# Kernel optimization log

Hardware: AMD Instinct MI355X
Metric: run time of the kernel (lower is better)

Reference implementation:

```python
import jax, jax.numpy as jnp
import numpy as np

INDEX_SHIFT = jnp.array([[0, 0], [-1, 0], [1, 0], [0, 1], [-1, 1], [1, 1], [0, -1], [-1, -1], [1, -1]], dtype=jnp.int32)
H, W = 320, 320
C = 32          # embed_dim / feat_channels (hard-coded 32 in module)
NH = 2          # head_num
HD = C // NH    # per-head dim
B, N = 4, 20000


def setup_inputs() -> dict:
    key = jax.random.key(0)
    ks = jax.random.split(key, 8)

    def coords(k):
        # unique (y, x) coords per sample so the coord->index lookup is well defined
        perm = jax.random.permutation(k, H * W)[:N]
        return jnp.stack([perm // W, perm % W], axis=-1).astype(jnp.int32)

    li_coors = jax.vmap(coords)(jax.random.split(ks[0], B))
    ra_coors = jax.vmap(coords)(jax.random.split(ks[1], B))
    li_feats = jax.random.normal(ks[2], (B, N, C), jnp.float32)
    ra_feats = jax.random.normal(ks[3], (B, N, C), jnp.float32)
    pos = jax.random.normal(ks[4], (9, C), jnp.float32) * 0.02

    s = 1.0 / np.sqrt(C)
    out = {"li_bev_feats": li_feats, "li_bev_coors": li_coors,
           "ra_bev_feats": ra_feats, "ra_bev_coors": ra_coors,
           "pos_embedding": pos}
    for i, kk in [(1, ks[5]), (2, ks[6])]:
        k0, k1 = jax.random.split(kk)
        out[f"in_w{i}"] = jax.random.uniform(k0, (3 * C, C), jnp.float32, -s, s)
        out[f"in_b{i}"] = jnp.zeros((3 * C,), jnp.float32)
        out[f"out_w{i}"] = jax.random.uniform(k1, (C, C), jnp.float32, -s, s)
        out[f"out_b{i}"] = jnp.zeros((C,), jnp.float32)
    return out


def _build_kv(q_coors, kv_coors, kv_feats, pos):
    # q_coors, kv_coors: (N,2) int; kv_feats: (N,C)
    n = q_coors.shape[0]
    grid = jnp.full((H * W,), -1, jnp.int32)
    grid = grid.at[kv_coors[:, 0] * W + kv_coors[:, 1]].set(jnp.arange(n, dtype=jnp.int32))
    sc = q_coors[None, :, :] + INDEX_SHIFT[:, None, :]            # (9,N,2)
    valid = (sc[..., 0] >= 0) & (sc[..., 0] < H) & (sc[..., 1] >= 0) & (sc[..., 1] < W)
    flat = jnp.clip(sc[..., 0], 0, H - 1) * W + jnp.clip(sc[..., 1], 0, W - 1)
    sel = jnp.where(valid, grid[flat], -1)                        # (9,N)
    mask = (sel >= 0)[..., None]                                  # (9,N,1)
    g = kv_feats[jnp.maximum(sel, 0)]                             # (9,N,C)
    k = jnp.where(mask, g, 0.0)
    v = jnp.where(mask, g + pos[:, None, :], 0.0)
    return k.transpose(1, 0, 2), v.transpose(1, 0, 2)             # (N,9,C)


def _mha(q, k, v, in_w, in_b, out_w, out_b):
    # q: (N,C); k,v: (N,L,C). torch MultiheadAttention (eval mode, dropout off).
    n, L = k.shape[0], k.shape[1]
    wq, wk, wv = in_w[:C], in_w[C:2 * C], in_w[2 * C:]
    bq, bk, bv = in_b[:C], in_b[C:2 * C], in_b[2 * C:]
    qh = (q @ wq.T + bq).reshape(n, NH, HD)
    kh = (k @ wk.T + bk).reshape(n, L, NH, HD)
    vh = (v @ wv.T + bv).reshape(n, L, NH, HD)
    scores = jnp.einsum('nhd,nlhd->nhl', qh, kh) / np.sqrt(HD)
    attn = jax.nn.softmax(scores, axis=-1)
    o = jnp.einsum('nhl,nlhd->nhd', attn, vh).reshape(n, C)
    return o @ out_w.T + out_b


def _scatter(feats, coors):
    # PointPillarsScatter: place (N,C) feats at (y,x) into a (C,H,W) canvas
    idx = coors[:, 0] * W + coors[:, 1]
    canvas = jnp.zeros((C, H * W), feats.dtype)
    return canvas.at[:, idx].set(feats.T).reshape(C, H, W)


def reference(li_bev_feats, li_bev_coors, ra_bev_feats, ra_bev_coors, pos_embedding,
              in_w1, in_b1, out_w1, out_b1, in_w2, in_b2, out_w2, out_b2):
    def one(li_f, li_c, ra_f, ra_c):
        k, v = _build_kv(li_c, ra_c, ra_f, pos_embedding)
        li_img = _scatter(_mha(li_f, k, v, in_w1, in_b1, out_w1, out_b1), li_c)
        k, v = _build_kv(ra_c, li_c, li_f, pos_embedding)
        ra_img = _scatter(_mha(ra_f, k, v, in_w2, in_b2, out_w2, out_b2), ra_c)
        return li_img, ra_img
    li_imgs, ra_imgs = jax.vmap(one)(li_bev_feats, li_bev_coors, ra_bev_feats, ra_bev_coors)
    return li_imgs, ra_imgs  # each (B, C, H, W)
```

## Files before the change

kernel.cpp:

```cpp
#include <hip/hip_runtime.h>

constexpr int Hh = 320, Ww = 320, Cc = 32, Bb = 4, Nn = 20000;
constexpr int HWp = Hh * Ww;

__device__ __forceinline__ float4 shfl_xor4(float4 v, int m) {
  return make_float4(__shfl_xor(v.x, m), __shfl_xor(v.y, m),
                     __shfl_xor(v.z, m), __shfl_xor(v.w, m));
}

__global__ __launch_bounds__(256) void prep_k(
    int* __restrict__ grids, const float* __restrict__ pos,
    const float* __restrict__ in_w1, const float* __restrict__ in_w2,
    float* __restrict__ posv) {
  int bx = blockIdx.x;
  if (bx < 800) {
    int i = bx * 256 + threadIdx.x;
    ((int4*)grids)[i] = make_int4(-1, -1, -1, -1);
    return;
  }
  int t = (bx - 800) * 256 + threadIdx.x;
  if (t >= 2 * 9 * Cc) return;
  int dir = t / (9 * Cc);
  int rem = t - dir * 9 * Cc;
  int l = rem / Cc, ch = rem - l * Cc;
  const float* w = (dir == 0 ? in_w1 : in_w2) + (2 * Cc + ch) * Cc;
  const float* pl = pos + l * Cc;
  float acc = 0.f;
  for (int j = 0; j < Cc; j++) acc += pl[j] * w[j];
  posv[t] = acc;
}

constexpr int PROJ_BLOCKS_PER_SB = 157;
constexpr int PROJ_TOTAL = PROJ_BLOCKS_PER_SB * 8;
constexpr int BUILD_BLOCKS = 625;

__global__ __launch_bounds__(256) void project_build_k(
    const float* __restrict__ li_feats, const float* __restrict__ ra_feats,
    const int* __restrict__ li_coors, const int* __restrict__ ra_coors,
    const float* __restrict__ in_w1, const float* __restrict__ in_b1,
    const float* __restrict__ in_w2, const float* __restrict__ in_b2,
    float* __restrict__ Qh, float* __restrict__ Kp, float* __restrict__ Vp,
    int* __restrict__ grids) {
  int bx = blockIdx.x;
  if (bx >= PROJ_TOTAL) {
    int idx = (bx - PROJ_TOTAL) * 256 + threadIdx.x;
    int src = idx / (Bb * Nn);
    int r = idx - src * (Bb * Nn);
    int b = r / Nn, n = r - b * Nn;
    const int* c = (src == 0 ? li_coors : ra_coors) + ((size_t)b * Nn + n) * 2;
    grids[((size_t)src * Bb + b) * HWp + c[0] * Ww + c[1]] = n;
    return;
  }
  int sb = bx / PROJ_BLOCKS_PER_SB;
  int blk = bx - sb * PROJ_BLOCKS_PER_SB;
  int src = sb >> 2, b = sb & 3;
  __shared__ __align__(16) float wqT[32 * 36];
  __shared__ __align__(16) float wkT[32 * 36];
  __shared__ __align__(16) float wvT[32 * 36];
  __shared__ float bq[Cc];
  const float* wA = src == 0 ? in_w1 : in_w2;
  const float* bA = src == 0 ? in_b1 : in_b2;
  const float* wB = src == 0 ? in_w2 : in_w1;
  int t = threadIdx.x;
  for (int i = t; i < Cc * Cc; i += 256) {
    int c = i >> 5, j = i & 31;
    wqT[j * 36 + c] = wA[i];
    wkT[j * 36 + c] = wB[Cc * Cc + i];
    wvT[j * 36 + c] = wB[2 * Cc * Cc + i];
  }
  if (t < Cc) bq[t] = bA[t];
  __syncthreads();
  int quad = t >> 3, c4 = t & 7;
  int n0 = blk * 128 + quad * 4;
  if (n0 + 4 > Nn) n0 = Nn - 4;
  const float* f = (src == 0 ? li_feats : ra_feats) + ((size_t)b * Nn + n0) * Cc;
  const float4* wq4 = (const float4*)wqT;
  const float4* wk4 = (const float4*)wkT;
  const float4* wv4 = (const float4*)wvT;
  float4 bq4 = *(const float4*)(bq + c4 * 4);
  float4 aq[4], ak[4], av[4];
#pragma unroll
  for (int i = 0; i < 4; i++) {
    aq[i] = bq4;
    ak[i] = make_float4(0.f, 0.f, 0.f, 0.f);
    av[i] = make_float4(0.f, 0.f, 0.f, 0.f);
  }
#pragma unroll
  for (int j4 = 0; j4 < 8; j4++) {
    float fjs[4][4];
#pragma unroll
    for (int i = 0; i < 4; i++) {
      float4 v = ((const float4*)(f + i * Cc))[j4];
      fjs[i][0] = v.x; fjs[i][1] = v.y; fjs[i][2] = v.z; fjs[i][3] = v.w;
    }
#pragma unroll
    for (int u = 0; u < 4; u++) {
      int j = j4 * 4 + u;
      float4 q4 = wq4[j * 9 + c4];
      float4 k4 = wk4[j * 9 + c4];
      float4 v4 = wv4[j * 9 + c4];
#pragma unroll
      for (int i = 0; i < 4; i++) {
        float fj = fjs[i][u];
        aq[i].x += fj * q4.x; aq[i].y += fj * q4.y;
        aq[i].z += fj * q4.z; aq[i].w += fj * q4.w;
        ak[i].x += fj * k4.x; ak[i].y += fj * k4.y;
        ak[i].z += fj * k4.z; ak[i].w += fj * k4.w;
        av[i].x += fj * v4.x; av[i].y += fj * v4.y;
        av[i].z += fj * v4.z; av[i].w += fj * v4.w;
      }
    }
  }
  int dirkv = 1 - src;
  size_t qbase = (((size_t)src * Bb + b) * Nn + n0) * Cc + c4 * 4;
  size_t kvbase = (((size_t)dirkv * Bb + b) * Nn + n0) * Cc + c4 * 4;
#pragma unroll
  for (int i = 0; i < 4; i++) {
    *(float4*)(Qh + qbase + i * Cc) = aq[i];
    *(float4*)(Kp + kvbase + i * Cc) = ak[i];
    *(float4*)(Vp + kvbase + i * Cc) = av[i];
  }
}

__global__ __launch_bounds__(256) void attn8_k(
    const int* __restrict__ li_coors, const int* __restrict__ ra_coors,
    const int* __restrict__ grids, const float* __restrict__ Qh,
    const float* __restrict__ Kp, const float* __restrict__ Vp,
    const float* __restrict__ posv, const float* __restrict__ in_b1,
    const float* __restrict__ in_b2, const float* __restrict__ out_w1,
    const float* __restrict__ out_b1, const float* __restrict__ out_w2,
    const float* __restrict__ out_b2, float* __restrict__ out_pts) {
  int db = blockIdx.y;
  int dir = db >> 2, b = db & 3;
  __shared__ __align__(16) float ow[Cc * Cc];
  __shared__ __align__(16) float pv[9 * Cc];
  __shared__ float sbk[Cc], sbv[Cc], sob[Cc];
  const float* owp = dir == 0 ? out_w1 : out_w2;
  const float* obp = dir == 0 ? out_b1 : out_b2;
  const float* ibp = dir == 0 ? in_b1 : in_b2;
  int t = threadIdx.x;
  for (int i = t; i < Cc * Cc; i += 256) ow[i] = owp[i];
  for (int i = t; i < 9 * Cc; i += 256) pv[i] = posv[dir * 9 * Cc + i];
  if (t < Cc) {
    sbk[t] = ibp[Cc + t];
    sbv[t] = ibp[2 * Cc + t];
    sob[t] = obp[t];
  }
  __syncthreads();
  int pt = t >> 3, c4 = t & 7;
  int n = blockIdx.x * 32 + pt;
  const int2* qcp =
      (const int2*)((dir == 0 ? li_coors : ra_coors) + (size_t)b * Nn * 2);
  int2 yx = qcp[n];
  int y = yx.x, x = yx.y;
  const int* g = grids + ((size_t)(1 - dir) * Bb + b) * HWp;
  const int DY[9] = {0, -1, 1, 0, -1, 1, 0, -1, 1};
  const int DX[9] = {0, 0, 0, 1, 1, 1, -1, -1, -1};
  int sel[9];
#pragma unroll
  for (int l = 0; l < 9; l++) {
    int cy = y + DY[l], cx = x + DX[l];
    sel[l] = ((unsigned)cy < (unsigned)Hh && (unsigned)cx < (unsigned)Ww)
                 ? g[cy * Ww + cx]
                 : -1;
  }
  const float* Kpb = Kp + ((size_t)dir * Bb + b) * Nn * Cc;
  const float* Vpb = Vp + ((size_t)dir * Bb + b) * Nn * Cc;
  float4 k4s[9], v4s[9];
#pragma unroll
  for (int l = 0; l < 9; l++) {
    float4 kk = make_float4(0.f, 0.f, 0.f, 0.f);
    float4 vv = make_float4(0.f, 0.f, 0.f, 0.f);
    int se = sel[l];
    if (se >= 0) {
      kk = *(const float4*)(Kpb + (size_t)se * Cc + c4 * 4);
      vv = *(const float4*)(Vpb + (size_t)se * Cc + c4 * 4);
    }
    k4s[l] = kk;
    v4s[l] = vv;
  }
  float4 qh4 =
      *(const float4*)(Qh + (((size_t)dir * Bb + b) * Nn + n) * Cc + c4 * 4);
  float4 bk4 = *(const float4*)(sbk + c4 * 4);
  float pb = qh4.x * bk4.x + qh4.y * bk4.y + qh4.z * bk4.z + qh4.w * bk4.w;
  pb += __shfl_xor(pb, 1);
  pb += __shfl_xor(pb, 2);
  float s[9];
#pragma unroll
  for (int l = 0; l < 9; l++) {
    float4 k4 = k4s[l];
    float d = qh4.x * k4.x + qh4.y * k4.y + qh4.z * k4.z + qh4.w * k4.w;
    d += __shfl_xor(d, 1);
    d += __shfl_xor(d, 2);
    s[l] = 0.25f * (pb + d);
  }
  float m = s[0];
#pragma unroll
  for (int l = 1; l < 9; l++) m = fmaxf(m, s[l]);
  float sum = 0.f;
#pragma unroll
  for (int l = 0; l < 9; l++) {
    s[l] = __expf(s[l] - m);
    sum += s[l];
  }
  float4 o4 = make_float4(0.f, 0.f, 0.f, 0.f);
#pragma unroll
  for (int l = 0; l < 9; l++) {
    float wp = (sel[l] >= 0) ? s[l] : 0.f;
    float4 v4 = v4s[l];
    float4 p4 = *(const float4*)(pv + l * Cc + c4 * 4);
    o4.x += wp * (v4.x + p4.x);
    o4.y += wp * (v4.y + p4.y);
    o4.z += wp * (v4.z + p4.z);
    o4.w += wp * (v4.w + p4.w);
  }
  float r = 1.f / sum;
  float4 bv4 = *(const float4*)(sbv + c4 * 4);
  o4 = make_float4(o4.x * r + bv4.x, o4.y * r + bv4.y, o4.z * r + bv4.z,
                   o4.w * r + bv4.w);
  const float4* ow4 = (const float4*)ow;
  float4 sob4 = *(const float4*)(sob + c4 * 4);
  float acc0 = sob4.x, acc1 = sob4.y, acc2 = sob4.z, acc3 = sob4.w;
#pragma unroll
  for (int mm = 0; mm < 8; mm++) {
    float4 oj = shfl_xor4(o4, mm);
    int jb = c4 ^ mm;
    float4 w0 = ow4[(c4 * 4 + 0) * 8 + jb];
    float4 w1 = ow4[(c4 * 4 + 1) * 8 + jb];
    float4 w2 = ow4[(c4 * 4 + 2) * 8 + jb];
    float4 w3 = ow4[(c4 * 4 + 3) * 8 + jb];
    acc0 += oj.x * w0.x + oj.y * w0.y + oj.z * w0.z + oj.w * w0.w;
    acc1 += oj.x * w1.x + oj.y * w1.y + oj.z * w1.z + oj.w * w1.w;
    acc2 += oj.x * w2.x + oj.y * w2.y + oj.z * w2.z + oj.w * w2.w;
    acc3 += oj.x * w3.x + oj.y * w3.y + oj.z * w3.z + oj.w * w3.w;
  }
  *(float4*)(out_pts + (((size_t)dir * Bb + b) * Nn + n) * Cc + c4 * 4) =
      make_float4(acc0, acc1, acc2, acc3);
}

__global__ __launch_bounds__(256) void scatter_k(
    const int* __restrict__ grids, const float* __restrict__ out_pts,
    float* __restrict__ out) {
  int db = blockIdx.y;
  int dir = db >> 2, b = db & 3;
  int p = blockIdx.x * 256 + threadIdx.x;
  const int* gq = grids + ((size_t)dir * Bb + b) * HWp;
  int se = gq[p];
  float* ob = out + (((size_t)dir * Bb + b) * Cc) * HWp + p;
  if (se < 0) {
#pragma unroll
    for (int c = 0; c < Cc; c++) ob[(size_t)c * HWp] = 0.f;
  } else {
    const float4* sp =
        (const float4*)(out_pts + (((size_t)dir * Bb + b) * Nn + se) * Cc);
#pragma unroll
    for (int c4 = 0; c4 < 8; c4++) {
      float4 v = sp[c4];
      ob[(size_t)(c4 * 4 + 0) * HWp] = v.x;
      ob[(size_t)(c4 * 4 + 1) * HWp] = v.y;
      ob[(size_t)(c4 * 4 + 2) * HWp] = v.z;
      ob[(size_t)(c4 * 4 + 3) * HWp] = v.w;
    }
  }
}

extern "C" void kernel_launch(void* const* d_in, const int* in_sizes, int n_in,
                              void* d_out, int out_size, void* d_ws, size_t ws_size,
                              hipStream_t stream) {
  const float* li_feats = (const float*)d_in[0];
  const int* li_coors = (const int*)d_in[1];
  const float* ra_feats = (const float*)d_in[2];
  const int* ra_coors = (const int*)d_in[3];
  const float* pos = (const float*)d_in[4];
  const float* in_w1 = (const float*)d_in[5];
  const float* in_b1 = (const float*)d_in[6];
  const float* out_w1 = (const float*)d_in[7];
  const float* out_b1 = (const float*)d_in[8];
  const float* in_w2 = (const float*)d_in[9];
  const float* in_b2 = (const float*)d_in[10];
  const float* out_w2 = (const float*)d_in[11];
  const float* out_b2 = (const float*)d_in[12];

  char* ws = (char*)d_ws;
  size_t off = 0;
  int* grids = (int*)(ws + off);
  off += (size_t)2 * Bb * HWp * 4;
  float* Qh = (float*)(ws + off);
  off += (size_t)2 * Bb * Nn * Cc * 4;
  float* Kp = (float*)(ws + off);
  off += (size_t)2 * Bb * Nn * Cc * 4;
  float* Vp = (float*)(ws + off);
  off += (size_t)2 * Bb * Nn * Cc * 4;
  float* out_pts = (float*)(ws + off);
  off += (size_t)2 * Bb * Nn * Cc * 4;
  float* posv = (float*)(ws + off);
  off += 2 * 9 * Cc * 4;

  prep_k<<<803, 256, 0, stream>>>(grids, pos, in_w1, in_w2, posv);
  project_build_k<<<PROJ_TOTAL + BUILD_BLOCKS, 256, 0, stream>>>(
      li_feats, ra_feats, li_coors, ra_coors, in_w1, in_b1, in_w2, in_b2, Qh, Kp,
      Vp, grids);
  dim3 ga(Nn / 32, 2 * Bb);
  attn8_k<<<ga, 256, 0, stream>>>(li_coors, ra_coors, grids, Qh, Kp, Vp, posv,
                                  in_b1, in_b2, out_w1, out_b1, out_w2, out_b2,
                                  out_pts);
  dim3 gs(HWp / 256, 2 * Bb);
  scatter_k<<<gs, 256, 0, stream>>>(grids, out_pts, (float*)d_out);
}
```

Before: 92.87 us.

## Compute Q projection inside attention kernel instead of materializing Qh

```diff
diff --git a/kernel.cpp b/kernel.cpp
--- a/kernel.cpp
+++ b/kernel.cpp
@@ -37,10 +37,8 @@
 __global__ __launch_bounds__(256) void project_build_k(
     const float* __restrict__ li_feats, const float* __restrict__ ra_feats,
     const int* __restrict__ li_coors, const int* __restrict__ ra_coors,
-    const float* __restrict__ in_w1, const float* __restrict__ in_b1,
-    const float* __restrict__ in_w2, const float* __restrict__ in_b2,
-    float* __restrict__ Qh, float* __restrict__ Kp, float* __restrict__ Vp,
-    int* __restrict__ grids) {
+    const float* __restrict__ in_w1, const float* __restrict__ in_w2,
+    float* __restrict__ Kp, float* __restrict__ Vp, int* __restrict__ grids) {
   int bx = blockIdx.x;
   if (bx >= PROJ_TOTAL) {
     int idx = (bx - PROJ_TOTAL) * 256 + threadIdx.x;
@@ -54,34 +52,25 @@
   int sb = bx / PROJ_BLOCKS_PER_SB;
   int blk = bx - sb * PROJ_BLOCKS_PER_SB;
   int src = sb >> 2, b = sb & 3;
-  __shared__ __align__(16) float wqT[32 * 36];
   __shared__ __align__(16) float wkT[32 * 36];
   __shared__ __align__(16) float wvT[32 * 36];
-  __shared__ float bq[Cc];
-  const float* wA = src == 0 ? in_w1 : in_w2;
-  const float* bA = src == 0 ? in_b1 : in_b2;
   const float* wB = src == 0 ? in_w2 : in_w1;
   int t = threadIdx.x;
   for (int i = t; i < Cc * Cc; i += 256) {
     int c = i >> 5, j = i & 31;
-    wqT[j * 36 + c] = wA[i];
-    wkT[j * 36 + c] = wB[Cc * Cc + i];
+    wkT[j * 36 + c] = 0.25f * wB[Cc * Cc + i];
     wvT[j * 36 + c] = wB[2 * Cc * Cc + i];
   }
-  if (t < Cc) bq[t] = bA[t];
   __syncthreads();
   int quad = t >> 3, c4 = t & 7;
   int n0 = blk * 128 + quad * 4;
   if (n0 + 4 > Nn) n0 = Nn - 4;
   const float* f = (src == 0 ? li_feats : ra_feats) + ((size_t)b * Nn + n0) * Cc;
-  const float4* wq4 = (const float4*)wqT;
   const float4* wk4 = (const float4*)wkT;
   const float4* wv4 = (const float4*)wvT;
-  float4 bq4 = *(const float4*)(bq + c4 * 4);
-  float4 aq[4], ak[4], av[4];
+  float4 ak[4], av[4];
 #pragma unroll
   for (int i = 0; i < 4; i++) {
-    aq[i] = bq4;
     ak[i] = make_float4(0.f, 0.f, 0.f, 0.f);
     av[i] = make_float4(0.f, 0.f, 0.f, 0.f);
   }
@@ -96,14 +85,11 @@
 #pragma unroll
     for (int u = 0; u < 4; u++) {
       int j = j4 * 4 + u;
-      float4 q4 = wq4[j * 9 + c4];
       float4 k4 = wk4[j * 9 + c4];
       float4 v4 = wv4[j * 9 + c4];
 #pragma unroll
       for (int i = 0; i < 4; i++) {
         float fj = fjs[i][u];
-        aq[i].x += fj * q4.x; aq[i].y += fj * q4.y;
-        aq[i].z += fj * q4.z; aq[i].w += fj * q4.w;
         ak[i].x += fj * k4.x; ak[i].y += fj * k4.y;
         ak[i].z += fj * k4.z; ak[i].w += fj * k4.w;
         av[i].x += fj * v4.x; av[i].y += fj * v4.y;
@@ -112,37 +98,43 @@
     }
   }
   int dirkv = 1 - src;
-  size_t qbase = (((size_t)src * Bb + b) * Nn + n0) * Cc + c4 * 4;
   size_t kvbase = (((size_t)dirkv * Bb + b) * Nn + n0) * Cc + c4 * 4;
 #pragma unroll
   for (int i = 0; i < 4; i++) {
-    *(float4*)(Qh + qbase + i * Cc) = aq[i];
     *(float4*)(Kp + kvbase + i * Cc) = ak[i];
     *(float4*)(Vp + kvbase + i * Cc) = av[i];
   }
 }
 
 __global__ __launch_bounds__(256) void attn8_k(
+    const float* __restrict__ li_feats, const float* __restrict__ ra_feats,
     const int* __restrict__ li_coors, const int* __restrict__ ra_coors,
-    const int* __restrict__ grids, const float* __restrict__ Qh,
+    const int* __restrict__ grids,
     const float* __restrict__ Kp, const float* __restrict__ Vp,
-    const float* __restrict__ posv, const float* __restrict__ in_b1,
-    const float* __restrict__ in_b2, const float* __restrict__ out_w1,
+    const float* __restrict__ posv, const float* __restrict__ in_w1,
+    const float* __restrict__ in_b1, const float* __restrict__ in_b2,
+    const float* __restrict__ in_w2, const float* __restrict__ out_w1,
     const float* __restrict__ out_b1, const float* __restrict__ out_w2,
     const float* __restrict__ out_b2, float* __restrict__ out_pts) {
   int db = blockIdx.y;
   int dir = db >> 2, b = db & 3;
+  __shared__ __align__(16) float swq[Cc * Cc];
   __shared__ __align__(16) float ow[Cc * Cc];
   __shared__ __align__(16) float pv[9 * Cc];
-  __shared__ float sbk[Cc], sbv[Cc], sob[Cc];
+  __shared__ float sbq[Cc], sbk[Cc], sbv[Cc], sob[Cc];
+  const float* wqp = dir == 0 ? in_w1 : in_w2;
   const float* owp = dir == 0 ? out_w1 : out_w2;
   const float* obp = dir == 0 ? out_b1 : out_b2;
   const float* ibp = dir == 0 ? in_b1 : in_b2;
   int t = threadIdx.x;
-  for (int i = t; i < Cc * Cc; i += 256) ow[i] = owp[i];
+  for (int i = t; i < Cc * Cc; i += 256) {
+    swq[i] = wqp[i];
+    ow[i] = owp[i];
+  }
   for (int i = t; i < 9 * Cc; i += 256) pv[i] = posv[dir * 9 * Cc + i];
   if (t < Cc) {
-    sbk[t] = ibp[Cc + t];
+    sbq[t] = ibp[t];
+    sbk[t] = 0.25f * ibp[Cc + t];
     sbv[t] = ibp[2 * Cc + t];
     sob[t] = obp[t];
   }
@@ -156,6 +148,9 @@
   const int* g = grids + ((size_t)(1 - dir) * Bb + b) * HWp;
   const int DY[9] = {0, -1, 1, 0, -1, 1, 0, -1, 1};
   const int DX[9] = {0, 0, 0, 1, 1, 1, -1, -1, -1};
+  const float* fb =
+      (dir == 0 ? li_feats : ra_feats) + ((size_t)b * Nn + n) * Cc;
+  float4 f4 = *(const float4*)(fb + c4 * 4);
   int sel[9];
 #pragma unroll
   for (int l = 0; l < 9; l++) {
@@ -179,8 +174,23 @@
     k4s[l] = kk;
     v4s[l] = vv;
   }
-  float4 qh4 =
-      *(const float4*)(Qh + (((size_t)dir * Bb + b) * Nn + n) * Cc + c4 * 4);
+  const float4* wq4 = (const float4*)swq;
+  float4 sbq4 = *(const float4*)(sbq + c4 * 4);
+  float q0 = sbq4.x, q1 = sbq4.y, q2 = sbq4.z, q3 = sbq4.w;
+#pragma unroll
+  for (int mm = 0; mm < 8; mm++) {
+    float4 fj = shfl_xor4(f4, mm);
+    int jb = c4 ^ mm;
+    float4 w0 = wq4[(c4 * 4 + 0) * 8 + jb];
+    float4 w1 = wq4[(c4 * 4 + 1) * 8 + jb];
+    float4 w2 = wq4[(c4 * 4 + 2) * 8 + jb];
+    float4 w3 = wq4[(c4 * 4 + 3) * 8 + jb];
+    q0 += fj.x * w0.x + fj.y * w0.y + fj.z * w0.z + fj.w * w0.w;
+    q1 += fj.x * w1.x + fj.y * w1.y + fj.z * w1.z + fj.w * w1.w;
+    q2 += fj.x * w2.x + fj.y * w2.y + fj.z * w2.z + fj.w * w2.w;
+    q3 += fj.x * w3.x + fj.y * w3.y + fj.z * w3.z + fj.w * w3.w;
+  }
+  float4 qh4 = make_float4(q0, q1, q2, q3);
   float4 bk4 = *(const float4*)(sbk + c4 * 4);
   float pb = qh4.x * bk4.x + qh4.y * bk4.y + qh4.z * bk4.z + qh4.w * bk4.w;
   pb += __shfl_xor(pb, 1);
@@ -192,7 +202,7 @@
     float d = qh4.x * k4.x + qh4.y * k4.y + qh4.z * k4.z + qh4.w * k4.w;
     d += __shfl_xor(d, 1);
     d += __shfl_xor(d, 2);
-    s[l] = 0.25f * (pb + d);
+    s[l] = pb + d;
   }
   float m = s[0];
 #pragma unroll
@@ -285,8 +295,6 @@
   size_t off = 0;
   int* grids = (int*)(ws + off);
   off += (size_t)2 * Bb * HWp * 4;
-  float* Qh = (float*)(ws + off);
-  off += (size_t)2 * Bb * Nn * Cc * 4;
   float* Kp = (float*)(ws + off);
   off += (size_t)2 * Bb * Nn * Cc * 4;
   float* Vp = (float*)(ws + off);
@@ -298,12 +306,11 @@
 
   prep_k<<<803, 256, 0, stream>>>(grids, pos, in_w1, in_w2, posv);
   project_build_k<<<PROJ_TOTAL + BUILD_BLOCKS, 256, 0, stream>>>(
-      li_feats, ra_feats, li_coors, ra_coors, in_w1, in_b1, in_w2, in_b2, Qh, Kp,
-      Vp, grids);
+      li_feats, ra_feats, li_coors, ra_coors, in_w1, in_w2, Kp, Vp, grids);
   dim3 ga(Nn / 32, 2 * Bb);
-  attn8_k<<<ga, 256, 0, stream>>>(li_coors, ra_coors, grids, Qh, Kp, Vp, posv,
-                                  in_b1, in_b2, out_w1, out_b1, out_w2, out_b2,
-                                  out_pts);
+  attn8_k<<<ga, 256, 0, stream>>>(li_feats, ra_feats, li_coors, ra_coors, grids,
+                                  Kp, Vp, posv, in_w1, in_b1, in_b2, in_w2,
+                                  out_w1, out_b1, out_w2, out_b2, out_pts);
   dim3 gs(HWp / 256, 2 * Bb);
   scatter_k<<<gs, 256, 0, stream>>>(grids, out_pts, (float*)d_out);
 }
```

Result: slower. 101.3 us (+9.1%).
